# Kernel tuning notes

Measured on AMD Instinct MI355X. Metric: run time of the kernel, lower is better.

Reference implementation:

```python
import jax, jax.numpy as jnp
import numpy as np

KH, KW = 3, 3
STRIDE = 1
OUT_C = 512


def im2col(x, kh, kw, stride):
    # x: [N, C, H, W] -> col: [C*kh*kw, N*oh*ow]  (row order: C major, then kh, kw)
    N, C, H, W = x.shape
    oh = (H - kh) // stride + 1
    ow = (W - kw) // stride + 1
    rows = jnp.arange(oh)[:, None] * stride + jnp.arange(kh)[None, :]  # [oh, kh]
    cols = jnp.arange(ow)[:, None] * stride + jnp.arange(kw)[None, :]  # [ow, kw]
    # gather windows: result [N, C, oh, kh, ow, kw]
    A = x[:, :, rows[:, :, None, None], cols[None, None, :, :]]
    # permute to (C, kh, kw, N, oh, ow) then flatten, matching torch permute(1,4,5,0,2,3)
    col = jnp.transpose(A, (1, 3, 5, 0, 2, 4)).reshape(C * kh * kw, N * oh * ow)
    return col, oh, ow


def setup_inputs() -> dict:
    key = jax.random.key(0)
    k1, k2, k3 = jax.random.split(key, 3)
    N, C, H, W = 16, 256, 32, 32
    K_sel = (C * KH * KW) // 2  # 1152 rows kept by the binary mask
    x = jax.random.normal(k1, (N, C, H, W), dtype=jnp.float32)
    weight = jax.random.normal(k2, (K_sel, OUT_C), dtype=jnp.float32) * 0.02
    idx = jnp.sort(jax.random.randint(k3, (K_sel,), 0, C * KH * KW, dtype=jnp.int32))
    return {"x": x, "weight": weight, "idx": idx}


def reference(x, weight, idx):
    N = x.shape[0]
    col, oh, ow = im2col(x, KH, KW, STRIDE)          # [C*kh*kw, N*oh*ow]
    x_tile = col[idx, :].T                            # gather masked rows -> [N*oh*ow, K_sel]
    conv_out = x_tile @ weight                        # [N*oh*ow, out_c]
    conv_out = conv_out.reshape(N, oh * ow, OUT_C)
    conv_out = jnp.transpose(conv_out, (0, 2, 1)).reshape(N, OUT_C, oh, ow)
    return conv_out
```

## Files before the change

kernel.cpp:

```cpp
#include <hip/hip_runtime.h>
#include <stdint.h>

#define N_IMG   16
#define C_IN    256
#define H_IN    32
#define W_IN    32
#define OH      30
#define OW      30
#define K_SEL   1152
#define OUTC    512
#define RY_TOT  (N_IMG * OH)
#define M_HAT   (RY_TOT * 32)
#define X_ELEMS (N_IMG * C_IN * H_IN * W_IN)
#define OUT_SP  (OH * OW)
#define CHW     (C_IN * H_IN * W_IN)

#define TO      128
#define TM      64
#define NMT     (M_HAT / TM)
#define NOT     (OUTC / TO)
#define BSTR    40
#define KITER   (K_SEL / 32)

typedef float f32x4  __attribute__((ext_vector_type(4)));
typedef short bf16x8 __attribute__((ext_vector_type(8)));

__device__ __forceinline__ unsigned short f2bf(float f) {
    unsigned int u = __float_as_uint(f);
    u += 0x7FFFu + ((u >> 16) & 1u);
    return (unsigned short)(u >> 16);
}

__global__ void prep_kernel(const int* __restrict__ idx, const float* __restrict__ w,
                            int* __restrict__ koff, unsigned short* __restrict__ wTf) {
    __shared__ float tile[32][33];
    const int bx = blockIdx.x, by = blockIdx.y, t = threadIdx.x;

    if (by == 0) {
        int k = bx * 256 + t;
        if (k < K_SEL) {
            int v = idx[k];
            int c = v / 9, rem = v - c * 9;
            int i = rem / 3, j = rem - i * 3;
            koff[k] = c * (H_IN * W_IN) + i * W_IN + j;
        }
    }
    const int s0 = bx * 32, o0 = by * 32;
    const int oc = t & 31, sg = t >> 5;
#pragma unroll
    for (int i = 0; i < 4; ++i) {
        int sl = sg * 4 + i;
        tile[sl][oc] = w[(s0 + sl) * OUTC + o0 + oc];
    }
    __syncthreads();
    const int ol = t >> 3, sq = t & 7;
    unsigned int u0 = (unsigned int)f2bf(tile[sq * 4 + 0][ol]) |
                      ((unsigned int)f2bf(tile[sq * 4 + 1][ol]) << 16);
    unsigned int u1 = (unsigned int)f2bf(tile[sq * 4 + 2][ol]) |
                      ((unsigned int)f2bf(tile[sq * 4 + 3][ol]) << 16);
    uint2 pk; pk.x = u0; pk.y = u1;
    const size_t fi =
        (((((size_t)(by >> 1) * KITER + bx) * 4 + ((by * 2 + (ol >> 4)) & 3)) * 64
          + (sq >> 1) * 16 + (ol & 15)) * 8) + (sq & 1) * 4;
    *reinterpret_cast<uint2*>(&wTf[fi]) = pk;
}

__global__ __launch_bounds__(256, 4)
void gemm_kernel(const unsigned short* __restrict__ wTf, const float* __restrict__ x,
                 const int* __restrict__ koff, float* __restrict__ out) {
    __shared__ __align__(16) unsigned short Bs[2][TM * BSTR];
    __shared__ int koS[K_SEL];

    const int t    = threadIdx.x;
    const int wave = t >> 6;
    const int lane = t & 63;
    const int quad = lane >> 4;
    const int lo   = lane & 15;

    const int bid = blockIdx.x;
    const int mt  = bid % NMT;
    const int ot  = bid / NMT;
    const int oBase = ot * TO;
    const int mBase = mt * TM;

    for (int i = t; i < K_SEL; i += 256) koS[i] = koff[i];

    const int xw  = t & 31;
    const int xwc = min(xw, 29);
    int basex[2];
#pragma unroll
    for (int ry = 0; ry < 2; ++ry) {
        int ryg = mt * 2 + ry;
        int n = ryg / 30, y = ryg - n * 30;
        basex[ry] = n * CHW + y * W_IN + xwc;
    }

    const int kq4 = t >> 5;
    const int ks  = kq4 * 4;

    const int ow64 = ot * 2 + (wave >> 1);
    const int idx0 = (wave * 2) & 3;
    const unsigned short* aP =
        wTf + ((size_t)ow64 * KITER * 4 + idx0) * 64 * 8 + (size_t)lane * 8;

    const unsigned short* bB[2] = {
        &Bs[0][lo * BSTR + quad * 8],
        &Bs[1][lo * BSTR + quad * 8] };
    unsigned short* bW[2] = {
        &Bs[0][xw * BSTR + ks],
        &Bs[1][xw * BSTR + ks] };

    __syncthreads();

    f32x4 acc[2][4] = {};
    bf16x8 aR[2][2];
    float v[2][2][4];

    {
        int4 k4 = *(const int4*)&koS[ks];
#pragma unroll
        for (int ry = 0; ry < 2; ++ry)
#pragma unroll
            for (int j = 0; j < 4; ++j)
                v[0][ry][j] = x[basex[ry] + ((const int*)&k4)[j]];
    }
    asm volatile("s_waitcnt vmcnt(0)" ::: "memory");
#pragma unroll
    for (int ry = 0; ry < 2; ++ry) {
        unsigned int u0 = (unsigned int)f2bf(v[0][ry][0]) |
                          ((unsigned int)f2bf(v[0][ry][1]) << 16);
        unsigned int u1 = (unsigned int)f2bf(v[0][ry][2]) |
                          ((unsigned int)f2bf(v[0][ry][3]) << 16);
        uint2 pk; pk.x = u0; pk.y = u1;
        *reinterpret_cast<uint2*>(bW[0] + ry * 32 * BSTR) = pk;
    }
#pragma unroll
    for (int ms = 0; ms < 2; ++ms)
        aR[0][ms] = *(const bf16x8*)(aP + (size_t)(0 * 4 + ms) * 64 * 8);
    {
        int4 k4 = *(const int4*)&koS[32 + ks];
#pragma unroll
        for (int ry = 0; ry < 2; ++ry)
#pragma unroll
            for (int j = 0; j < 4; ++j)
                v[1][ry][j] = x[basex[ry] + ((const int*)&k4)[j]];
    }
    asm volatile("s_waitcnt lgkmcnt(0)" ::: "memory");
    __builtin_amdgcn_s_barrier();

#pragma unroll 2
    for (int kt = 0; kt < KITER; ++kt) {
        const int p = kt & 1, q = p ^ 1;

        bf16x8 b[4];
#pragma unroll
        for (int ns = 0; ns < 4; ++ns)
            b[ns] = *(const bf16x8*)(bB[p] + ns * 16 * BSTR);

        {
            const int k1 = (kt + 1 < KITER ? kt + 1 : KITER - 1);
#pragma unroll
            for (int ms = 0; ms < 2; ++ms)
                aR[q][ms] = *(const bf16x8*)(aP + (size_t)(k1 * 4 + ms) * 64 * 8);
        }
        {
            const int k2 = (kt + 2 < KITER ? kt + 2 : KITER - 1) * 32;
            int4 k4 = *(const int4*)&koS[k2 + ks];
#pragma unroll
            for (int ry = 0; ry < 2; ++ry)
#pragma unroll
                for (int j = 0; j < 4; ++j)
                    v[p][ry][j] = x[basex[ry] + ((const int*)&k4)[j]];
        }
        asm volatile("s_waitcnt vmcnt(10)" ::: "memory");
        asm volatile("s_waitcnt lgkmcnt(0)" ::: "memory");
        __builtin_amdgcn_sched_barrier(0);
#pragma unroll
        for (int ry = 0; ry < 2; ++ry) {
            unsigned int u0 = (unsigned int)f2bf(v[q][ry][0]) |
                              ((unsigned int)f2bf(v[q][ry][1]) << 16);
            unsigned int u1 = (unsigned int)f2bf(v[q][ry][2]) |
                              ((unsigned int)f2bf(v[q][ry][3]) << 16);
            uint2 pk; pk.x = u0; pk.y = u1;
            *reinterpret_cast<uint2*>(bW[q] + ry * 32 * BSTR) = pk;
        }
#pragma unroll
        for (int ms = 0; ms < 2; ++ms)
#pragma unroll
            for (int ns = 0; ns < 4; ++ns)
                acc[ms][ns] = __builtin_amdgcn_mfma_f32_16x16x32_bf16(
                    aR[p][ms], b[ns], acc[ms][ns], 0, 0, 0);
        asm volatile("s_waitcnt lgkmcnt(0)" ::: "memory");
        __builtin_amdgcn_s_barrier();
    }

#pragma unroll
    for (int ns = 0; ns < 4; ++ns) {
        const int mh  = mBase + ns * 16 + lo;
        const int xwe = mh & 31;
        const int ryg = mh >> 5;
        const int n = ryg / 30, y = ryg - n * 30;
        if (xwe < OW) {
            const size_t ob = (size_t)n * (OUTC * OUT_SP) + (size_t)y * OW + xwe;
#pragma unroll
            for (int ms = 0; ms < 2; ++ms) {
                const int o0 = oBase + wave * 32 + ms * 16 + quad * 4;
#pragma unroll
                for (int r = 0; r < 4; ++r)
                    out[ob + (size_t)(o0 + r) * OUT_SP] = acc[ms][ns][r];
            }
        }
    }
}

extern "C" void kernel_launch(void* const* d_in, const int* in_sizes, int n_in,
                              void* d_out, int out_size, void* d_ws, size_t ws_size,
                              hipStream_t stream) {
    const float* x   = (const float*)d_in[0];
    const float* w   = (const float*)d_in[1];
    const int*   idx = (const int*)d_in[2];
    float*       out = (float*)d_out;

    char* ws = (char*)d_ws;
    int*            koff = (int*)ws;
    unsigned short* wTf  = (unsigned short*)(ws + 4608);

    prep_kernel<<<dim3(K_SEL / 32, OUTC / 32), dim3(256), 0, stream>>>(idx, w, koff, wTf);
    gemm_kernel<<<dim3(NMT * NOT), dim3(256), 0, stream>>>(wTf, x, koff, out);
}
```

Measured before the change: 104.1 us.

## Pre-pack im2col activations to bf16 buffer and stream via global_load_lds

Adds a path that materializes the gathered im2col activation tile as bf16 in MFMA-ready fragment order, in a prep kernel that also packs the weights. The GEMM kernel then loads each B tile with direct global-to-LDS 16-byte loads instead of doing per-element gathers and bf16 conversion inside the main loop. This is meant to remove scattered gather latency and conversion work from the GEMM's critical path. In exchange it writes and re-reads a roughly 35 MB intermediate buffer, which costs memory traffic. The old path is kept as a fallback when the workspace is too small.

```diff
diff --git a/kernel.cpp b/kernel.cpp
--- a/kernel.cpp
+++ b/kernel.cpp
@@ -22,6 +22,11 @@
 #define BSTR    40
 #define KITER   (K_SEL / 32)
 
+#define NPACK   (NMT * KITER)
+#define NPREPW  (36 * 16)
+#define WTF_BYTES 1179648u
+#define BF_BYTES  35389440u
+
 typedef float f32x4  __attribute__((ext_vector_type(4)));
 typedef short bf16x8 __attribute__((ext_vector_type(8)));
 
@@ -31,11 +36,167 @@
     return (unsigned short)(u >> 16);
 }
 
-__global__ void prep_kernel(const int* __restrict__ idx, const float* __restrict__ w,
-                            int* __restrict__ koff, unsigned short* __restrict__ wTf) {
+__device__ __forceinline__ void gl_lds16(const void* g, void* lds) {
+    __builtin_amdgcn_global_load_lds(
+        (const __attribute__((address_space(1))) unsigned int*)g,
+        (__attribute__((address_space(3))) unsigned int*)lds,
+        16, 0, 0);
+}
+
+
+__global__ void prepA_kernel(const int* __restrict__ idx, const float* __restrict__ w,
+                             const float* __restrict__ x,
+                             unsigned short* __restrict__ wTf,
+                             unsigned short* __restrict__ Bf) {
+    __shared__ float tile[32][33];
+    const int bid = blockIdx.x, t = threadIdx.x;
+
+    if (bid < NPACK) {
+        const int mt = bid / KITER, kt = bid - mt * KITER;
+        const int lane = t & 63, ns = t >> 6;
+        const int quad = lane >> 4, lo = lane & 15;
+        const int m  = ns * 16 + lo;
+        const int ry = m >> 5, xw = m & 31;
+        const int ryg = mt * 2 + ry;
+        const int n = ryg / 30, y = ryg - n * 30;
+        const int base = n * CHW + y * W_IN + min(xw, 29);
+        unsigned int uu[4];
+#pragma unroll
+        for (int jp = 0; jp < 4; ++jp) {
+            unsigned short ua, ub;
+            {
+                int k = kt * 32 + quad * 8 + jp * 2;
+                int v = idx[k];
+                int c = v / 9, rem = v - c * 9;
+                int i = rem / 3, j2 = rem - i * 3;
+                ua = f2bf(x[base + c * (H_IN * W_IN) + i * W_IN + j2]);
+            }
+            {
+                int k = kt * 32 + quad * 8 + jp * 2 + 1;
+                int v = idx[k];
+                int c = v / 9, rem = v - c * 9;
+                int i = rem / 3, j2 = rem - i * 3;
+                ub = f2bf(x[base + c * (H_IN * W_IN) + i * W_IN + j2]);
+            }
+            uu[jp] = (unsigned int)ua | ((unsigned int)ub << 16);
+        }
+        uint4 pk; pk.x = uu[0]; pk.y = uu[1]; pk.z = uu[2]; pk.w = uu[3];
+        *reinterpret_cast<uint4*>(&Bf[(size_t)bid * 2048 + t * 8]) = pk;
+    } else {
+        const int b = bid - NPACK;
+        const int bx = b % 36, by = b / 36;
+        const int s0 = bx * 32, o0 = by * 32;
+        const int oc = t & 31, sg = t >> 5;
+#pragma unroll
+        for (int i = 0; i < 4; ++i) {
+            int sl = sg * 4 + i;
+            tile[sl][oc] = w[(s0 + sl) * OUTC + o0 + oc];
+        }
+        __syncthreads();
+        const int ol = t >> 3, sq = t & 7;
+        unsigned int u0 = (unsigned int)f2bf(tile[sq * 4 + 0][ol]) |
+                          ((unsigned int)f2bf(tile[sq * 4 + 1][ol]) << 16);
+        unsigned int u1 = (unsigned int)f2bf(tile[sq * 4 + 2][ol]) |
+                          ((unsigned int)f2bf(tile[sq * 4 + 3][ol]) << 16);
+        uint2 pk; pk.x = u0; pk.y = u1;
+        const size_t fi =
+            (((((size_t)(by >> 1) * KITER + bx) * 4 + ((by * 2 + (ol >> 4)) & 3)) * 64
+              + (sq >> 1) * 16 + (ol & 15)) * 8) + (sq & 1) * 4;
+        *reinterpret_cast<uint2*>(&wTf[fi]) = pk;
+    }
+}
+
+__global__ __launch_bounds__(256, 4)
+void gemmA_kernel(const unsigned short* __restrict__ wTf,
+                  const unsigned short* __restrict__ Bf,
+                  float* __restrict__ out) {
+    __shared__ __align__(16) unsigned short Bs[2][2048];
+
+    const int t    = threadIdx.x;
+    const int wave = t >> 6;
+    const int lane = t & 63;
+    const int quad = lane >> 4;
+    const int lo   = lane & 15;
+
+    const int bid = blockIdx.x;
+    const int mt  = bid % NMT;
+    const int ot  = bid / NMT;
+    const int oBase = ot * TO;
+    const int mBase = mt * TM;
+
+    const int ow64 = ot * 2 + (wave >> 1);
+    const int idx0 = (wave * 2) & 3;
+    const unsigned short* aP =
+        wTf + ((size_t)ow64 * KITER * 4 + idx0) * 512 + (size_t)lane * 8;
+    const unsigned short* bfP =
+        Bf + (size_t)mt * KITER * 2048 + wave * 512 + (size_t)lane * 8;
+
+    unsigned short* ldst0 = &Bs[0][wave * 512];
+    unsigned short* ldst1 = &Bs[1][wave * 512];
+    const unsigned short* bRd0 = &Bs[0][lane * 8];
+    const unsigned short* bRd1 = &Bs[1][lane * 8];
+
+    f32x4 acc[2][4] = {};
+    bf16x8 aR[2][2];
+
+    gl_lds16(bfP, ldst0);
+    aR[0][0] = *(const bf16x8*)(aP);
+    aR[0][1] = *(const bf16x8*)(aP + 512);
+    asm volatile("s_waitcnt vmcnt(2)" ::: "memory");
+    __builtin_amdgcn_s_barrier();
+
+#pragma unroll 2
+    for (int kt = 0; kt < KITER; ++kt) {
+        const int p = kt & 1, q = p ^ 1;
+        const int k1 = (kt + 1 < KITER ? kt + 1 : KITER - 1);
+
+        gl_lds16(bfP + (size_t)k1 * 2048, q ? ldst1 : ldst0);
+        aR[q][0] = *(const bf16x8*)(aP + (size_t)(k1 * 4) * 512);
+        aR[q][1] = *(const bf16x8*)(aP + (size_t)(k1 * 4 + 1) * 512);
+
+        bf16x8 b[4];
+        const unsigned short* br = p ? bRd1 : bRd0;
+#pragma unroll
+        for (int ns = 0; ns < 4; ++ns)
+            b[ns] = *(const bf16x8*)(br + ns * 512);
+        asm volatile("s_waitcnt lgkmcnt(0)" ::: "memory");
+        __builtin_amdgcn_sched_barrier(0);
+        asm volatile("s_waitcnt vmcnt(3)" ::: "memory");
+
+#pragma unroll
+        for (int ms = 0; ms < 2; ++ms)
+#pragma unroll
+            for (int ns = 0; ns < 4; ++ns)
+                acc[ms][ns] = __builtin_amdgcn_mfma_f32_16x16x32_bf16(
+                    aR[p][ms], b[ns], acc[ms][ns], 0, 0, 0);
+
+        asm volatile("s_waitcnt vmcnt(2)" ::: "memory");
+        __builtin_amdgcn_s_barrier();
+    }
+
+#pragma unroll
+    for (int ns = 0; ns < 4; ++ns) {
+        const int mh  = mBase + ns * 16 + lo;
+        const int xwe = mh & 31;
+        const int ryg = mh >> 5;
+        const int n = ryg / 30, y = ryg - n * 30;
+        if (xwe < OW) {
+            const size_t ob = (size_t)n * (OUTC * OUT_SP) + (size_t)y * OW + xwe;
+#pragma unroll
+            for (int ms = 0; ms < 2; ++ms) {
+                const int o0 = oBase + wave * 32 + ms * 16 + quad * 4;
+#pragma unroll
+                for (int r = 0; r < 4; ++r)
+                    out[ob + (size_t)(o0 + r) * OUT_SP] = acc[ms][ns][r];
+            }
+        }
+    }
+}
+
+__global__ void prepB_kernel(const int* __restrict__ idx, const float* __restrict__ w,
+                             int* __restrict__ koff, unsigned short* __restrict__ wTf) {
     __shared__ float tile[32][33];
     const int bx = blockIdx.x, by = blockIdx.y, t = threadIdx.x;
-
     if (by == 0) {
         int k = bx * 256 + t;
         if (k < K_SEL) {
@@ -66,27 +227,16 @@
 }
 
 __global__ __launch_bounds__(256, 4)
-void gemm_kernel(const unsigned short* __restrict__ wTf, const float* __restrict__ x,
-                 const int* __restrict__ koff, float* __restrict__ out) {
+void gemmB_kernel(const unsigned short* __restrict__ wTf, const float* __restrict__ x,
+                  const int* __restrict__ koff, float* __restrict__ out) {
     __shared__ __align__(16) unsigned short Bs[2][TM * BSTR];
     __shared__ int koS[K_SEL];
-
-    const int t    = threadIdx.x;
-    const int wave = t >> 6;
-    const int lane = t & 63;
-    const int quad = lane >> 4;
-    const int lo   = lane & 15;
-
-    const int bid = blockIdx.x;
-    const int mt  = bid % NMT;
-    const int ot  = bid / NMT;
-    const int oBase = ot * TO;
-    const int mBase = mt * TM;
-
+    const int t = threadIdx.x, wave = t >> 6, lane = t & 63;
+    const int quad = lane >> 4, lo = lane & 15;
+    const int bid = blockIdx.x, mt = bid % NMT, ot = bid / NMT;
+    const int oBase = ot * TO, mBase = mt * TM;
     for (int i = t; i < K_SEL; i += 256) koS[i] = koff[i];
-
-    const int xw  = t & 31;
-    const int xwc = min(xw, 29);
+    const int xw = t & 31, xwc = min(xw, 29);
     int basex[2];
 #pragma unroll
     for (int ry = 0; ry < 2; ++ry) {
@@ -94,28 +244,19 @@
         int n = ryg / 30, y = ryg - n * 30;
         basex[ry] = n * CHW + y * W_IN + xwc;
     }
-
-    const int kq4 = t >> 5;
-    const int ks  = kq4 * 4;
-
+    const int kq4 = t >> 5, ks = kq4 * 4;
     const int ow64 = ot * 2 + (wave >> 1);
     const int idx0 = (wave * 2) & 3;
     const unsigned short* aP =
-        wTf + ((size_t)ow64 * KITER * 4 + idx0) * 64 * 8 + (size_t)lane * 8;
-
+        wTf + ((size_t)ow64 * KITER * 4 + idx0) * 512 + (size_t)lane * 8;
     const unsigned short* bB[2] = {
-        &Bs[0][lo * BSTR + quad * 8],
-        &Bs[1][lo * BSTR + quad * 8] };
+        &Bs[0][lo * BSTR + quad * 8], &Bs[1][lo * BSTR + quad * 8] };
     unsigned short* bW[2] = {
-        &Bs[0][xw * BSTR + ks],
-        &Bs[1][xw * BSTR + ks] };
-
+        &Bs[0][xw * BSTR + ks], &Bs[1][xw * BSTR + ks] };
     __syncthreads();
-
     f32x4 acc[2][4] = {};
     bf16x8 aR[2][2];
     float v[2][2][4];
-
     {
         int4 k4 = *(const int4*)&koS[ks];
 #pragma unroll
@@ -136,7 +277,7 @@
     }
 #pragma unroll
     for (int ms = 0; ms < 2; ++ms)
-        aR[0][ms] = *(const bf16x8*)(aP + (size_t)(0 * 4 + ms) * 64 * 8);
+        aR[0][ms] = *(const bf16x8*)(aP + (size_t)ms * 512);
     {
         int4 k4 = *(const int4*)&koS[32 + ks];
 #pragma unroll
@@ -147,21 +288,18 @@
     }
     asm volatile("s_waitcnt lgkmcnt(0)" ::: "memory");
     __builtin_amdgcn_s_barrier();
-
 #pragma unroll 2
     for (int kt = 0; kt < KITER; ++kt) {
         const int p = kt & 1, q = p ^ 1;
-
         bf16x8 b[4];
 #pragma unroll
         for (int ns = 0; ns < 4; ++ns)
             b[ns] = *(const bf16x8*)(bB[p] + ns * 16 * BSTR);
-
         {
             const int k1 = (kt + 1 < KITER ? kt + 1 : KITER - 1);
 #pragma unroll
             for (int ms = 0; ms < 2; ++ms)
-                aR[q][ms] = *(const bf16x8*)(aP + (size_t)(k1 * 4 + ms) * 64 * 8);
+                aR[q][ms] = *(const bf16x8*)(aP + (size_t)(k1 * 4 + ms) * 512);
         }
         {
             const int k2 = (kt + 2 < KITER ? kt + 2 : KITER - 1) * 32;
@@ -193,7 +331,6 @@
         asm volatile("s_waitcnt lgkmcnt(0)" ::: "memory");
         __builtin_amdgcn_s_barrier();
     }
-
 #pragma unroll
     for (int ns = 0; ns < 4; ++ns) {
         const int mh  = mBase + ns * 16 + lo;
@@ -220,11 +357,19 @@
     const float* w   = (const float*)d_in[1];
     const int*   idx = (const int*)d_in[2];
     float*       out = (float*)d_out;
-
     char* ws = (char*)d_ws;
-    int*            koff = (int*)ws;
-    unsigned short* wTf  = (unsigned short*)(ws + 4608);
-
-    prep_kernel<<<dim3(K_SEL / 32, OUTC / 32), dim3(256), 0, stream>>>(idx, w, koff, wTf);
-    gemm_kernel<<<dim3(NMT * NOT), dim3(256), 0, stream>>>(wTf, x, koff, out);
-}
+
+    if (ws_size >= (size_t)WTF_BYTES + BF_BYTES) {
+        unsigned short* wTf = (unsigned short*)ws;
+        unsigned short* Bf  = (unsigned short*)(ws + WTF_BYTES);
+        prepA_kernel<<<dim3(NPACK + NPREPW), dim3(256), 0, stream>>>(
+            idx, w, x, wTf, Bf);
+        gemmA_kernel<<<dim3(NMT * NOT), dim3(256), 0, stream>>>(wTf, Bf, out);
+    } else {
+        int*            koff = (int*)ws;
+        unsigned short* wTf  = (unsigned short*)(ws + 4608);
+        prepB_kernel<<<dim3(K_SEL / 32, OUTC / 32), dim3(256), 0, stream>>>(
+            idx, w, koff, wTf);
+        gemmB_kernel<<<dim3(NMT * NOT), dim3(256), 0, stream>>>(wTf, x, koff, out);
+    }
+}
```

Measured after the change: 103.7 us. No clear change (-0.4%).
